# Optimization experiments

Measured on AMD Instinct MI355X. Metric: run time of the kernel, lower is better.

Reference implementation:

```python
import jax, jax.numpy as jnp
import numpy as np

N_NODES = 50000
N_EDGES = 800000
D_FEAT = 64


def setup_inputs() -> dict:
    key = jax.random.key(0)
    k_x, k_e, k_w = jax.random.split(key, 3)
    x = jax.random.normal(k_x, (N_NODES, D_FEAT), dtype=jnp.float32)
    edge_index = jax.random.randint(k_e, (2, N_EDGES), 0, N_NODES, dtype=jnp.int64)
    # message MLP params (phi_Theta): single linear + ReLU
    W = jax.random.normal(k_w, (D_FEAT, D_FEAT), dtype=jnp.float32) / np.sqrt(D_FEAT)
    b = jnp.zeros((D_FEAT,), dtype=jnp.float32)
    return {"x": x, "edge_index": edge_index, "W": W, "b": b}


def reference(x, edge_index, W, b):
    # flow = source_to_target: messages flow from edge_index[0] (j) to edge_index[1] (i)
    src = edge_index[0]  # j: source nodes (gather)
    dst = edge_index[1]  # i: target nodes (scatter index)
    n_nodes = x.shape[0]
    # __collect__: index_select gather of source node features -> x_j [E, D]
    x_j = x[src]
    # message: per-edge MLP  phi(x_j) = relu(x_j W + b)
    msg = jax.nn.relu(jnp.einsum('ed,df->ef', x_j, W) + b)
    # aggregate: scatter-add into target nodes (aggr='add', dim_size = size_i)
    out = jax.ops.segment_sum(msg, dst, num_segments=n_nodes)
    # update: identity
    return out
```

## Files before the change

kernel.cpp:

```cpp
#include <hip/hip_runtime.h>
#include <hip/hip_bf16.h>

#define D 64
#define CAP 32
#define EUNROLL 4
#define OVF_CAP 16384

__device__ __forceinline__ float bf2f(unsigned short u) {
    return __uint_as_float((unsigned int)u << 16);
}
__device__ __forceinline__ unsigned short f2bf(float f) {
    unsigned int u = __float_as_uint(f);
    unsigned int r = (u + 0x7fffu + ((u >> 16) & 1u)) >> 16;
    return (unsigned short)r;
}

__global__ __launch_bounds__(256) void node_mlp_kernel(
    const float* __restrict__ x, const float* __restrict__ W,
    const float* __restrict__ b, unsigned short* __restrict__ m0,
    unsigned short* __restrict__ m1, int* __restrict__ cnt,
    int* __restrict__ ovf_cnt, int n_nodes) {
    for (int i = blockIdx.x * blockDim.x + threadIdx.x; i < n_nodes;
         i += gridDim.x * blockDim.x) cnt[i] = 0;
    if (blockIdx.x == 0 && threadIdx.x == 0) *ovf_cnt = 0;

    const int lane = threadIdx.x & 63;
    const int l31 = lane & 31;
    unsigned short* mp = (lane < 32) ? m0 : m1;
    float w[D];
    #pragma unroll
    for (int k = 0; k < D; ++k) w[k] = W[k * D + lane];
    const float bias = b[lane];

    const int wave = (blockIdx.x * blockDim.x + threadIdx.x) >> 6;
    const int nwaves = (gridDim.x * blockDim.x) >> 6;

    for (int row = wave; row < n_nodes; row += nwaves) {
        const float4* xr = (const float4*)(x + (size_t)row * D);
        float acc = bias;
        #pragma unroll
        for (int kk = 0; kk < D / 4; ++kk) {
            float4 xv = xr[kk];
            acc = fmaf(xv.x, w[4 * kk + 0], acc);
            acc = fmaf(xv.y, w[4 * kk + 1], acc);
            acc = fmaf(xv.z, w[4 * kk + 2], acc);
            acc = fmaf(xv.w, w[4 * kk + 3], acc);
        }
        mp[(size_t)row * 32 + l31] = f2bf(fmaxf(acc, 0.0f));
    }
}

__global__ __launch_bounds__(256) void append_kernel(
    const int* __restrict__ src, const int* __restrict__ dst,
    int* __restrict__ cnt, unsigned short* __restrict__ slots,
    int* __restrict__ ovf_cnt, unsigned int* __restrict__ ovf, int n_edges) {
    const int base = blockIdx.x * 256 * EUNROLL + threadIdx.x;
    int s[EUNROLL], d[EUNROLL], pos[EUNROLL];
    bool ok[EUNROLL];
    #pragma unroll
    for (int i = 0; i < EUNROLL; ++i) {
        int e = base + i * 256;
        ok[i] = (e < n_edges);
        s[i] = ok[i] ? src[e] : 0;
        d[i] = ok[i] ? dst[e] : 0;
    }
    #pragma unroll
    for (int i = 0; i < EUNROLL; ++i)
        pos[i] = ok[i] ? atomicAdd(&cnt[d[i]], 1) : CAP;
    #pragma unroll
    for (int i = 0; i < EUNROLL; ++i) {
        if (!ok[i]) continue;
        if (pos[i] < CAP) {
            slots[(size_t)d[i] * CAP + pos[i]] = (unsigned short)s[i];
        } else {
            int op = atomicAdd(ovf_cnt, 1);
            if (op < OVF_CAP)
                ovf[op] = ((unsigned int)d[i] << 16) | (unsigned int)s[i];
        }
    }
}

__global__ __launch_bounds__(256) void gather_pass_kernel(
    const unsigned short* __restrict__ slots, const int* __restrict__ cnt,
    const unsigned short* __restrict__ mplane,
    const int* __restrict__ ovf_cnt, const unsigned int* __restrict__ ovf,
    float* __restrict__ out, int n_nodes, int col0) {
    const int lane = threadIdx.x & 63;
    const int l31 = lane & 31;
    const int wave = (blockIdx.x * 256 + threadIdx.x) >> 6;
    const int node = wave * 2 + ((lane >> 5) & 1);
    if (node >= n_nodes) return;

    const int c = cnt[node];
    const int cc = min(c, CAP);
    unsigned int idx = (unsigned int)slots[(size_t)node * CAP + l31];
    const int bsel = lane & 32;

    float acc = 0.0f;
    int k = 0;
    for (; k + 4 <= cc; k += 4) {
        unsigned int s0 = __shfl(idx, bsel + k + 0);
        unsigned int s1 = __shfl(idx, bsel + k + 1);
        unsigned int s2 = __shfl(idx, bsel + k + 2);
        unsigned int s3 = __shfl(idx, bsel + k + 3);
        float v0 = bf2f(mplane[(size_t)s0 * 32 + l31]);
        float v1 = bf2f(mplane[(size_t)s1 * 32 + l31]);
        float v2 = bf2f(mplane[(size_t)s2 * 32 + l31]);
        float v3 = bf2f(mplane[(size_t)s3 * 32 + l31]);
        acc += (v0 + v1) + (v2 + v3);
    }
    for (; k < cc; ++k) {
        unsigned int s = __shfl(idx, bsel + k);
        acc += bf2f(mplane[(size_t)s * 32 + l31]);
    }
    if (c > CAP) {
        int oc = min(*ovf_cnt, OVF_CAP);
        for (int i = 0; i < oc; ++i) {
            unsigned int e = ovf[i];
            if ((int)(e >> 16) == node)
                acc += bf2f(mplane[(size_t)(e & 0xFFFFu) * 32 + l31]);
        }
    }
    out[(size_t)node * D + col0 + l31] = acc;
}

__global__ __launch_bounds__(256) void edge_scatter_kernel(
    const int* __restrict__ src, const int* __restrict__ dst,
    const unsigned short* __restrict__ m0, const unsigned short* __restrict__ m1,
    float* __restrict__ out, int n_edges) {
    long long t = (long long)blockIdx.x * blockDim.x + threadIdx.x;
    int e = (int)(t >> 4);
    if (e >= n_edges) return;
    int c = (int)(t & 15) << 2;
    int s = src[e];
    int d = dst[e];
    const unsigned short* mp = (c < 32) ? m0 : m1;
    const ushort4 v = *(const ushort4*)(mp + (size_t)s * 32 + (c & 31));
    float* o = out + (size_t)d * D + c;
    atomicAdd(o + 0, bf2f(v.x));
    atomicAdd(o + 1, bf2f(v.y));
    atomicAdd(o + 2, bf2f(v.z));
    atomicAdd(o + 3, bf2f(v.w));
}

static inline size_t align_up(size_t v, size_t a) { return (v + a - 1) & ~(a - 1); }

extern "C" void kernel_launch(void* const* d_in, const int* in_sizes, int n_in,
                              void* d_out, int out_size, void* d_ws, size_t ws_size,
                              hipStream_t stream) {
    const float* x = (const float*)d_in[0];
    const int* edge_index = (const int*)d_in[1];
    const float* W = (const float*)d_in[2];
    const float* b = (const float*)d_in[3];
    float* out = (float*)d_out;

    const int n_nodes = in_sizes[0] / D;
    const int n_edges = in_sizes[1] / 2;
    const int* src = edge_index;
    const int* dst = edge_index + n_edges;

    size_t off = 0;
    unsigned short* m0 = (unsigned short*)((char*)d_ws + off);
    off = align_up(off + (size_t)n_nodes * 32 * sizeof(unsigned short), 256);
    unsigned short* m1 = (unsigned short*)((char*)d_ws + off);
    off = align_up(off + (size_t)n_nodes * 32 * sizeof(unsigned short), 256);
    int* cnt = (int*)((char*)d_ws + off);
    off = align_up(off + (size_t)n_nodes * sizeof(int), 256);
    unsigned short* slots = (unsigned short*)((char*)d_ws + off);
    off = align_up(off + (size_t)n_nodes * CAP * sizeof(unsigned short), 256);
    int* ovf_cnt = (int*)((char*)d_ws + off);
    off = align_up(off + sizeof(int), 256);
    unsigned int* ovf = (unsigned int*)((char*)d_ws + off);
    off = align_up(off + (size_t)OVF_CAP * sizeof(unsigned int), 256);
    const size_t needed = off;

    node_mlp_kernel<<<512, 256, 0, stream>>>(x, W, b, m0, m1, cnt, ovf_cnt, n_nodes);

    if (ws_size >= needed && n_nodes <= 65536) {
        const int ablocks = (n_edges + 256 * EUNROLL - 1) / (256 * EUNROLL);
        append_kernel<<<ablocks, 256, 0, stream>>>(src, dst, cnt, slots,
                                                   ovf_cnt, ovf, n_edges);
        const int gblocks = (n_nodes + 7) / 8;
        gather_pass_kernel<<<gblocks, 256, 0, stream>>>(
            slots, cnt, m0, ovf_cnt, ovf, out, n_nodes, 0);
        gather_pass_kernel<<<gblocks, 256, 0, stream>>>(
            slots, cnt, m1, ovf_cnt, ovf, out, n_nodes, 32);
    } else {
        hipMemsetAsync(d_out, 0, (size_t)out_size * sizeof(float), stream);
        long long total_threads = (long long)n_edges * 16;
        int scat_blocks = (int)((total_threads + 255) / 256);
        edge_scatter_kernel<<<scat_blocks, 256, 0, stream>>>(src, dst, m0, m1,
                                                             out, n_edges);
    }
}
```

Before: 169.9 us.

## Shard edge append by destination and merge gather passes into one launch

The append kernel now launches 8 shards of blocks. Each shard scans a chunk of edges and handles only those whose destination node falls in its residue class mod 8. The intent is to give atomics and slot writes better locality, likely by spreading them across memory channels or XCDs. The cost is that every shard re-reads the dst array, so index reads grow about eightfold. Separately, the two per-plane gather launches are merged into one launch of twice the blocks, which removes one launch and its tail.

```diff
diff --git a/kernel.cpp b/kernel.cpp
--- a/kernel.cpp
+++ b/kernel.cpp
@@ -3,8 +3,8 @@
 
 #define D 64
 #define CAP 32
-#define EUNROLL 4
 #define OVF_CAP 16384
+#define NSHARD 8
 
 __device__ __forceinline__ float bf2f(unsigned short u) {
     return __uint_as_float((unsigned int)u << 16);
@@ -53,41 +53,42 @@
 __global__ __launch_bounds__(256) void append_kernel(
     const int* __restrict__ src, const int* __restrict__ dst,
     int* __restrict__ cnt, unsigned short* __restrict__ slots,
-    int* __restrict__ ovf_cnt, unsigned int* __restrict__ ovf, int n_edges) {
-    const int base = blockIdx.x * 256 * EUNROLL + threadIdx.x;
-    int s[EUNROLL], d[EUNROLL], pos[EUNROLL];
-    bool ok[EUNROLL];
-    #pragma unroll
-    for (int i = 0; i < EUNROLL; ++i) {
-        int e = base + i * 256;
-        ok[i] = (e < n_edges);
-        s[i] = ok[i] ? src[e] : 0;
-        d[i] = ok[i] ? dst[e] : 0;
-    }
-    #pragma unroll
-    for (int i = 0; i < EUNROLL; ++i)
-        pos[i] = ok[i] ? atomicAdd(&cnt[d[i]], 1) : CAP;
-    #pragma unroll
-    for (int i = 0; i < EUNROLL; ++i) {
-        if (!ok[i]) continue;
-        if (pos[i] < CAP) {
-            slots[(size_t)d[i] * CAP + pos[i]] = (unsigned short)s[i];
+    int* __restrict__ ovf_cnt, unsigned int* __restrict__ ovf,
+    int n_edges, int blocks_per_shard) {
+    const int shard = blockIdx.x & (NSHARD - 1);
+    const int p = blockIdx.x >> 3;
+    const int chunk = (n_edges + blocks_per_shard - 1) / blocks_per_shard;
+    const int beg = p * chunk;
+    const int end = min(beg + chunk, n_edges);
+
+    for (int e = beg + (int)threadIdx.x; e < end; e += 256) {
+        int d = dst[e];
+        if ((d & (NSHARD - 1)) != shard) continue;
+        int s = src[e];
+        int pos = atomicAdd(&cnt[d], 1);
+        if (pos < CAP) {
+            slots[(size_t)d * CAP + pos] = (unsigned short)s;
         } else {
             int op = atomicAdd(ovf_cnt, 1);
             if (op < OVF_CAP)
-                ovf[op] = ((unsigned int)d[i] << 16) | (unsigned int)s[i];
+                ovf[op] = ((unsigned int)d << 16) | (unsigned int)s;
         }
     }
 }
 
 __global__ __launch_bounds__(256) void gather_pass_kernel(
     const unsigned short* __restrict__ slots, const int* __restrict__ cnt,
-    const unsigned short* __restrict__ mplane,
+    const unsigned short* __restrict__ m0, const unsigned short* __restrict__ m1,
     const int* __restrict__ ovf_cnt, const unsigned int* __restrict__ ovf,
-    float* __restrict__ out, int n_nodes, int col0) {
+    float* __restrict__ out, int n_nodes, int gblocks) {
+    const int plane = ((int)blockIdx.x >= gblocks) ? 1 : 0;
+    const int blk = (int)blockIdx.x - plane * gblocks;
+    const unsigned short* mplane = plane ? m1 : m0;
+    const int col0 = plane * 32;
+
     const int lane = threadIdx.x & 63;
     const int l31 = lane & 31;
-    const int wave = (blockIdx.x * 256 + threadIdx.x) >> 6;
+    const int wave = (blk * 256 + (int)threadIdx.x) >> 6;
     const int node = wave * 2 + ((lane >> 5) & 1);
     if (node >= n_nodes) return;
 
@@ -177,14 +178,12 @@
     node_mlp_kernel<<<512, 256, 0, stream>>>(x, W, b, m0, m1, cnt, ovf_cnt, n_nodes);
 
     if (ws_size >= needed && n_nodes <= 65536) {
-        const int ablocks = (n_edges + 256 * EUNROLL - 1) / (256 * EUNROLL);
-        append_kernel<<<ablocks, 256, 0, stream>>>(src, dst, cnt, slots,
-                                                   ovf_cnt, ovf, n_edges);
+        const int blocks_per_shard = 128;
+        append_kernel<<<blocks_per_shard * NSHARD, 256, 0, stream>>>(
+            src, dst, cnt, slots, ovf_cnt, ovf, n_edges, blocks_per_shard);
         const int gblocks = (n_nodes + 7) / 8;
-        gather_pass_kernel<<<gblocks, 256, 0, stream>>>(
-            slots, cnt, m0, ovf_cnt, ovf, out, n_nodes, 0);
-        gather_pass_kernel<<<gblocks, 256, 0, stream>>>(
-            slots, cnt, m1, ovf_cnt, ovf, out, n_nodes, 32);
+        gather_pass_kernel<<<gblocks * 2, 256, 0, stream>>>(
+            slots, cnt, m0, m1, ovf_cnt, ovf, out, n_nodes, gblocks);
     } else {
         hipMemsetAsync(d_out, 0, (size_t)out_size * sizeof(float), stream);
         long long total_threads = (long long)n_edges * 16;
```

Result: faster. 158.3 us (-6.8%).
